# Kernel tuning notes

Measured on AMD Instinct MI355X. Metric: run time of the kernel, lower is better.

The kernel has to match this reference:

```python
import jax, jax.numpy as jnp
import numpy as np

A = -0.75  # bicubic kernel coefficient (matches torch/TF bicubic)

def _cubic_weights(t):
    """Cubic-convolution weights for the 4 taps at offsets -1,0,1,2; t in [0,1)."""
    def w_in(s):   # |s| <= 1
        return ((A + 2.0) * s - (A + 3.0)) * s * s + 1.0
    def w_out(s):  # 1 < |s| < 2
        return ((A * s - 5.0 * A) * s + 8.0 * A) * s - 4.0 * A
    return jnp.stack([w_out(t + 1.0), w_in(t), w_in(1.0 - t), w_out(2.0 - t)], axis=-1)

def setup_inputs() -> dict:
    key = jax.random.key(0)
    k1, k2 = jax.random.split(key)
    B, Hf, Wf, C = 8, 160, 160, 64
    H, W = 1280, 1280
    x = jax.random.normal(k1, (B, Hf, Wf, C), dtype=jnp.float32)
    # keypoint positions in original-image pixel coords [0, W-1] x [0, H-1]
    u = jax.random.uniform(k2, (B, 4096, 2), dtype=jnp.float32)
    pos = u * jnp.array([W - 1, H - 1], dtype=jnp.float32)
    return {"x": x, "pos": pos, "H": H, "W": W}

def reference(x, pos, H, W):
    """Bicubic grid_sample at sparse positions; align_corners=False, zeros padding.
    x: [B,Hf,Wf,C], pos: [B,N,2] (x,y) in original HxW pixel coords -> [B,N,C]."""
    B, Hf, Wf, C = x.shape
    # normalize to [-1,1] using the ORIGINAL resolution (H, W)
    gx = 2.0 * pos[..., 0] / (W - 1) - 1.0
    gy = 2.0 * pos[..., 1] / (H - 1) - 1.0
    # unnormalize to feature-map coords (align_corners=False)
    ix = ((gx + 1.0) * Wf - 1.0) * 0.5
    iy = ((gy + 1.0) * Hf - 1.0) * 0.5
    fx = jnp.floor(ix); fy = jnp.floor(iy)
    tx = ix - fx; ty = iy - fy
    offs = jnp.arange(-1, 3, dtype=jnp.int32)            # 4 taps
    xi = fx.astype(jnp.int32)[..., None] + offs           # [B,N,4]
    yi = fy.astype(jnp.int32)[..., None] + offs           # [B,N,4]
    wx = _cubic_weights(tx)                                # [B,N,4]
    wy = _cubic_weights(ty)                                # [B,N,4]
    # zeros padding: mask out-of-bounds taps
    vx = (xi >= 0) & (xi < Wf)
    vy = (yi >= 0) & (yi < Hf)
    xc = jnp.clip(xi, 0, Wf - 1)
    yc = jnp.clip(yi, 0, Hf - 1)
    lin = yc[:, :, :, None] * Wf + xc[:, :, None, :]       # [B,N,4,4] (i=y tap, j=x tap)
    xflat = x.reshape(B, Hf * Wf, C)
    vals = jax.vmap(lambda xb, ib: xb[ib])(xflat, lin)     # [B,N,4,4,C]
    m = (vy[:, :, :, None] & vx[:, :, None, :]).astype(x.dtype)
    vals = vals * m[..., None]
    return jnp.einsum('bnijc,bni,bnj->bnc', vals, wy, wx)  # [B,N,C]
```

## Files before the change

kernel.cpp:

```cpp
#include <hip/hip_runtime.h>
#include <hip/hip_bf16.h>

constexpr int B  = 8;
constexpr int Hf = 160;
constexpr int Wf = 160;
constexpr int C  = 64;
constexpr int N  = 4096;
constexpr int NXCD = 8;

typedef float f32x4 __attribute__((ext_vector_type(4)));
typedef float f32x2 __attribute__((ext_vector_type(2)));

__device__ __forceinline__ void cubic_weights(float t, float w[4]) {
    const float A = -0.75f;
    float s;
    s = t + 1.0f;
    w[0] = ((A * s - 5.0f * A) * s + 8.0f * A) * s - 4.0f * A;
    s = t;
    w[1] = ((A + 2.0f) * s - (A + 3.0f)) * s * s + 1.0f;
    s = 1.0f - t;
    w[2] = ((A + 2.0f) * s - (A + 3.0f)) * s * s + 1.0f;
    s = 2.0f - t;
    w[3] = ((A * s - 5.0f * A) * s + 8.0f * A) * s - 4.0f * A;
}

__global__ __launch_bounds__(256)
void interp_sparse_bicubic(const float* __restrict__ x,
                           const float* __restrict__ pos,
                           const int* __restrict__ Hp,
                           const int* __restrict__ Wp,
                           float* __restrict__ out) {
    int blk  = blockIdx.x;
    int b    = blk & (NXCD - 1);
    int slot = blk >> 3;
    int q    = threadIdx.x & 15;
    int pib  = threadIdx.x >> 4;
    int n    = slot * 16 + pib;
    int pnt  = b * N + n;

    f32x2 p = *reinterpret_cast<const f32x2*>(pos + (size_t)pnt * 2);
    float Wo = (float)Wp[0];
    float Ho = (float)Hp[0];

    float gx = 2.0f * p.x / (Wo - 1.0f) - 1.0f;
    float gy = 2.0f * p.y / (Ho - 1.0f) - 1.0f;
    float ix = ((gx + 1.0f) * (float)Wf - 1.0f) * 0.5f;
    float iy = ((gy + 1.0f) * (float)Hf - 1.0f) * 0.5f;

    float fx = floorf(ix), fy = floorf(iy);
    float tx = ix - fx,    ty = iy - fy;
    int x0 = (int)fx, y0 = (int)fy;

    float wx[4], wy[4];
    cubic_weights(tx, wx);
    cubic_weights(ty, wy);

    int yc[4], xc[4];
    #pragma unroll
    for (int i = 0; i < 4; ++i) {
        int yi = y0 - 1 + i;
        wy[i] = (yi >= 0 && yi < Hf) ? wy[i] : 0.0f;
        yc[i] = min(max(yi, 0), Hf - 1);
        int xj = x0 - 1 + i;
        wx[i] = (xj >= 0 && xj < Wf) ? wx[i] : 0.0f;
        xc[i] = min(max(xj, 0), Wf - 1);
    }

    const float* xb = x + (size_t)b * (Hf * Wf * C) + q * 4;

    f32x4 v[4][4];
    #pragma unroll
    for (int i = 0; i < 4; ++i) {
        const float* row = xb + (size_t)yc[i] * (Wf * C);
        #pragma unroll
        for (int j = 0; j < 4; ++j) {
            v[i][j] = *reinterpret_cast<const f32x4*>(row + (size_t)xc[j] * C);
        }
    }

    f32x4 acc = {0.f, 0.f, 0.f, 0.f};
    #pragma unroll
    for (int i = 0; i < 4; ++i) {
        #pragma unroll
        for (int j = 0; j < 4; ++j) {
            float w = wy[i] * wx[j];
            acc.x = fmaf(w, v[i][j].x, acc.x);
            acc.y = fmaf(w, v[i][j].y, acc.y);
            acc.z = fmaf(w, v[i][j].z, acc.z);
            acc.w = fmaf(w, v[i][j].w, acc.w);
        }
    }

    f32x4* op = reinterpret_cast<f32x4*>(out + (size_t)pnt * C + q * 4);
    __builtin_nontemporal_store(acc, op);
}

extern "C" void kernel_launch(void* const* d_in, const int* in_sizes, int n_in,
                              void* d_out, int out_size, void* d_ws, size_t ws_size,
                              hipStream_t stream) {
    const float* x   = (const float*)d_in[0];
    const float* pos = (const float*)d_in[1];
    const int*   Hp  = (const int*)d_in[2];
    const int*   Wp  = (const int*)d_in[3];
    float* out = (float*)d_out;

    int grid = B * (N / 16);
    interp_sparse_bicubic<<<grid, 256, 0, stream>>>(x, pos, Hp, Wp, out);
}
```

Before: 14.76 us.

## Spatially bin keypoints via counting sort before bicubic gather for cache locality

Adds a preprocessing pipeline (memset, count, scan, scatter) that sorts keypoints into 8x8-pixel feature-map tiles per batch, then runs the interpolation over the sorted order and writes results back to the original indices. The aim is to make neighbouring blocks gather overlapping 4x4 footprints so L2/cache reuse improves. It costs four extra launches plus atomics, and falls back to the direct kernel when the workspace is too small.

```diff
diff --git a/kernel.cpp b/kernel.cpp
--- a/kernel.cpp
+++ b/kernel.cpp
@@ -7,6 +7,17 @@
 constexpr int C  = 64;
 constexpr int N  = 4096;
 constexpr int NXCD = 8;
+
+constexpr int TPX  = 8;
+constexpr int TPS  = 20;
+constexpr int BINS = TPS * TPS;
+
+constexpr int WS_CNT  = 0;
+constexpr int WS_CUR  = B * BINS;
+constexpr int WS_BASE = 2 * B * BINS;
+constexpr int WS_IDX  = 3 * B * BINS;
+constexpr int WS_POS  = WS_IDX + B * N;
+constexpr size_t WS_NEED = (size_t)(WS_POS + 2 * B * N) * 4;
 
 typedef float f32x4 __attribute__((ext_vector_type(4)));
 typedef float f32x2 __attribute__((ext_vector_type(2)));
@@ -24,29 +35,145 @@
     w[3] = ((A * s - 5.0f * A) * s + 8.0f * A) * s - 4.0f * A;
 }
 
-__global__ __launch_bounds__(256)
-void interp_sparse_bicubic(const float* __restrict__ x,
-                           const float* __restrict__ pos,
-                           const int* __restrict__ Hp,
-                           const int* __restrict__ Wp,
-                           float* __restrict__ out) {
+__device__ __forceinline__ int point_bin(f32x2 p, float Wo, float Ho) {
+    float gx = 2.0f * p.x / (Wo - 1.0f) - 1.0f;
+    float gy = 2.0f * p.y / (Ho - 1.0f) - 1.0f;
+    float ix = ((gx + 1.0f) * (float)Wf - 1.0f) * 0.5f;
+    float iy = ((gy + 1.0f) * (float)Hf - 1.0f) * 0.5f;
+    int x0 = min(max((int)floorf(ix), 0), Wf - 1);
+    int y0 = min(max((int)floorf(iy), 0), Hf - 1);
+    return (y0 / TPX) * TPS + (x0 / TPX);
+}
+
+__global__ __launch_bounds__(256)
+void count_bins(const float* __restrict__ pos, const int* __restrict__ Hp,
+                const int* __restrict__ Wp, int* __restrict__ ws) {
+    int pid = blockIdx.x * blockDim.x + threadIdx.x;
+    if (pid >= B * N) return;
+    int b = pid >> 12;
+    f32x2 p = *reinterpret_cast<const f32x2*>(pos + (size_t)pid * 2);
+    int bin = point_bin(p, (float)Wp[0], (float)Hp[0]);
+    atomicAdd(&ws[WS_CNT + b * BINS + bin], 1);
+}
+
+__global__ __launch_bounds__(512)
+void scan_bins(int* __restrict__ ws) {
+    int w = threadIdx.x >> 6;
+    int l = threadIdx.x & 63;
+    int carry = 0;
+    for (int c = 0; c < (BINS + 63) / 64; ++c) {
+        int idx = c * 64 + l;
+        int v = (idx < BINS) ? ws[WS_CNT + w * BINS + idx] : 0;
+        int incl = v;
+        #pragma unroll
+        for (int off = 1; off < 64; off <<= 1) {
+            int o = __shfl_up(incl, off);
+            if (l >= off) incl += o;
+        }
+        if (idx < BINS) ws[WS_BASE + w * BINS + idx] = carry + incl - v;
+        carry += __shfl(incl, 63);
+    }
+}
+
+__global__ __launch_bounds__(256)
+void scatter_points(const float* __restrict__ pos, const int* __restrict__ Hp,
+                    const int* __restrict__ Wp, int* __restrict__ ws) {
+    int pid = blockIdx.x * blockDim.x + threadIdx.x;
+    if (pid >= B * N) return;
+    int b = pid >> 12, n = pid & (N - 1);
+    f32x2 p = *reinterpret_cast<const f32x2*>(pos + (size_t)pid * 2);
+    int bin = point_bin(p, (float)Wp[0], (float)Hp[0]);
+    int slot = ws[WS_BASE + b * BINS + bin]
+             + atomicAdd(&ws[WS_CUR + b * BINS + bin], 1);
+    int g = b * N + slot;
+    ws[WS_IDX + g] = n;
+    reinterpret_cast<f32x2*>(ws + WS_POS)[g] = p;
+}
+
+__global__ __launch_bounds__(256)
+void interp_sorted(const float* __restrict__ x, const int* __restrict__ ws,
+                   const int* __restrict__ Hp, const int* __restrict__ Wp,
+                   float* __restrict__ out) {
+    int g    = blockIdx.x;
+    int b    = g & (NXCD - 1);
+    int slot = g >> 3;
+    int q    = threadIdx.x & 15;
+    int pib  = threadIdx.x >> 4;
+    int i    = slot * 16 + pib;
+
+    f32x2 p = reinterpret_cast<const f32x2*>(ws + WS_POS)[b * N + i];
+    int   n = ws[WS_IDX + b * N + i];
+    float Wo = (float)Wp[0], Ho = (float)Hp[0];
+
+    float gx = 2.0f * p.x / (Wo - 1.0f) - 1.0f;
+    float gy = 2.0f * p.y / (Ho - 1.0f) - 1.0f;
+    float ix = ((gx + 1.0f) * (float)Wf - 1.0f) * 0.5f;
+    float iy = ((gy + 1.0f) * (float)Hf - 1.0f) * 0.5f;
+
+    float fx = floorf(ix), fy = floorf(iy);
+    float tx = ix - fx,    ty = iy - fy;
+    int x0 = (int)fx, y0 = (int)fy;
+
+    float wx[4], wy[4];
+    cubic_weights(tx, wx);
+    cubic_weights(ty, wy);
+
+    int yc[4], xc[4];
+    #pragma unroll
+    for (int k = 0; k < 4; ++k) {
+        int yi = y0 - 1 + k;
+        wy[k] = (yi >= 0 && yi < Hf) ? wy[k] : 0.0f;
+        yc[k] = min(max(yi, 0), Hf - 1);
+        int xj = x0 - 1 + k;
+        wx[k] = (xj >= 0 && xj < Wf) ? wx[k] : 0.0f;
+        xc[k] = min(max(xj, 0), Wf - 1);
+    }
+
+    const float* xb = x + (size_t)b * (Hf * Wf * C) + q * 4;
+
+    f32x4 v[4][4];
+    #pragma unroll
+    for (int k = 0; k < 4; ++k) {
+        const float* row = xb + (size_t)yc[k] * (Wf * C);
+        #pragma unroll
+        for (int j = 0; j < 4; ++j)
+            v[k][j] = *reinterpret_cast<const f32x4*>(row + (size_t)xc[j] * C);
+    }
+
+    f32x4 acc = {0.f, 0.f, 0.f, 0.f};
+    #pragma unroll
+    for (int k = 0; k < 4; ++k) {
+        #pragma unroll
+        for (int j = 0; j < 4; ++j) {
+            float w = wy[k] * wx[j];
+            acc.x = fmaf(w, v[k][j].x, acc.x);
+            acc.y = fmaf(w, v[k][j].y, acc.y);
+            acc.z = fmaf(w, v[k][j].z, acc.z);
+            acc.w = fmaf(w, v[k][j].w, acc.w);
+        }
+    }
+
+    f32x4* op = reinterpret_cast<f32x4*>(out + ((size_t)b * N + n) * C + q * 4);
+    __builtin_nontemporal_store(acc, op);
+}
+
+__global__ __launch_bounds__(256)
+void interp_direct(const float* __restrict__ x, const float* __restrict__ pos,
+                   const int* __restrict__ Hp, const int* __restrict__ Wp,
+                   float* __restrict__ out) {
     int blk  = blockIdx.x;
     int b    = blk & (NXCD - 1);
     int slot = blk >> 3;
     int q    = threadIdx.x & 15;
     int pib  = threadIdx.x >> 4;
-    int n    = slot * 16 + pib;
-    int pnt  = b * N + n;
+    int pnt  = b * N + slot * 16 + pib;
 
     f32x2 p = *reinterpret_cast<const f32x2*>(pos + (size_t)pnt * 2);
-    float Wo = (float)Wp[0];
-    float Ho = (float)Hp[0];
-
+    float Wo = (float)Wp[0], Ho = (float)Hp[0];
     float gx = 2.0f * p.x / (Wo - 1.0f) - 1.0f;
     float gy = 2.0f * p.y / (Ho - 1.0f) - 1.0f;
     float ix = ((gx + 1.0f) * (float)Wf - 1.0f) * 0.5f;
     float iy = ((gy + 1.0f) * (float)Hf - 1.0f) * 0.5f;
-
     float fx = floorf(ix), fy = floorf(iy);
     float tx = ix - fx,    ty = iy - fy;
     int x0 = (int)fx, y0 = (int)fy;
@@ -57,40 +184,36 @@
 
     int yc[4], xc[4];
     #pragma unroll
-    for (int i = 0; i < 4; ++i) {
-        int yi = y0 - 1 + i;
-        wy[i] = (yi >= 0 && yi < Hf) ? wy[i] : 0.0f;
-        yc[i] = min(max(yi, 0), Hf - 1);
-        int xj = x0 - 1 + i;
-        wx[i] = (xj >= 0 && xj < Wf) ? wx[i] : 0.0f;
-        xc[i] = min(max(xj, 0), Wf - 1);
+    for (int k = 0; k < 4; ++k) {
+        int yi = y0 - 1 + k;
+        wy[k] = (yi >= 0 && yi < Hf) ? wy[k] : 0.0f;
+        yc[k] = min(max(yi, 0), Hf - 1);
+        int xj = x0 - 1 + k;
+        wx[k] = (xj >= 0 && xj < Wf) ? wx[k] : 0.0f;
+        xc[k] = min(max(xj, 0), Wf - 1);
     }
 
     const float* xb = x + (size_t)b * (Hf * Wf * C) + q * 4;
-
     f32x4 v[4][4];
     #pragma unroll
-    for (int i = 0; i < 4; ++i) {
-        const float* row = xb + (size_t)yc[i] * (Wf * C);
+    for (int k = 0; k < 4; ++k) {
+        const float* row = xb + (size_t)yc[k] * (Wf * C);
+        #pragma unroll
+        for (int j = 0; j < 4; ++j)
+            v[k][j] = *reinterpret_cast<const f32x4*>(row + (size_t)xc[j] * C);
+    }
+    f32x4 acc = {0.f, 0.f, 0.f, 0.f};
+    #pragma unroll
+    for (int k = 0; k < 4; ++k) {
         #pragma unroll
         for (int j = 0; j < 4; ++j) {
-            v[i][j] = *reinterpret_cast<const f32x4*>(row + (size_t)xc[j] * C);
+            float w = wy[k] * wx[j];
+            acc.x = fmaf(w, v[k][j].x, acc.x);
+            acc.y = fmaf(w, v[k][j].y, acc.y);
+            acc.z = fmaf(w, v[k][j].z, acc.z);
+            acc.w = fmaf(w, v[k][j].w, acc.w);
         }
     }
-
-    f32x4 acc = {0.f, 0.f, 0.f, 0.f};
-    #pragma unroll
-    for (int i = 0; i < 4; ++i) {
-        #pragma unroll
-        for (int j = 0; j < 4; ++j) {
-            float w = wy[i] * wx[j];
-            acc.x = fmaf(w, v[i][j].x, acc.x);
-            acc.y = fmaf(w, v[i][j].y, acc.y);
-            acc.z = fmaf(w, v[i][j].z, acc.z);
-            acc.w = fmaf(w, v[i][j].w, acc.w);
-        }
-    }
-
     f32x4* op = reinterpret_cast<f32x4*>(out + (size_t)pnt * C + q * 4);
     __builtin_nontemporal_store(acc, op);
 }
@@ -104,6 +227,16 @@
     const int*   Wp  = (const int*)d_in[3];
     float* out = (float*)d_out;
 
-    int grid = B * (N / 16);
-    interp_sparse_bicubic<<<grid, 256, 0, stream>>>(x, pos, Hp, Wp, out);
-}
+    if (ws_size < WS_NEED) {
+        interp_direct<<<B * (N / 16), 256, 0, stream>>>(x, pos, Hp, Wp, out);
+        return;
+    }
+
+    int* ws = (int*)d_ws;
+    hipMemsetAsync(ws, 0, (size_t)2 * B * BINS * sizeof(int), stream);
+
+    count_bins<<<(B * N) / 256, 256, 0, stream>>>(pos, Hp, Wp, ws);
+    scan_bins<<<1, 512, 0, stream>>>(ws);
+    scatter_points<<<(B * N) / 256, 256, 0, stream>>>(pos, Hp, Wp, ws);
+    interp_sorted<<<B * (N / 16), 256, 0, stream>>>(x, ws, Hp, Wp, out);
+}
```

New measurement: 30.56 us. 107% more time.
